# Performance work log

Measured on AMD Instinct MI355X. Metric: run time of the kernel, lower is better.

The kernel has to match this reference:

```python
import jax, jax.numpy as jnp
import numpy as np

H, W, CIN = 448, 608, 64
D = (128, 128, 1024)  # depth list from the module
SCALE = 0.02

def setup_inputs() -> dict:
    key = jax.random.key(0)
    ks = jax.random.split(key, 9)
    f32 = jnp.float32
    return {
        "x":  jax.random.normal(ks[0], (1, CIN, H, W), f32),
        "w1": jax.random.normal(ks[1], (D[0], CIN, 3, 3), f32) * SCALE,
        "b1": jax.random.normal(ks[2], (D[0],), f32) * SCALE,
        "w2": jax.random.normal(ks[3], (H, D[1], D[0]), f32) * SCALE,
        "b2": jax.random.normal(ks[4], (H, D[1]), f32) * SCALE,
        "w3": jax.random.normal(ks[5], (H, D[2], D[1]), f32) * SCALE,
        "b3": jax.random.normal(ks[6], (H, D[2]), f32) * SCALE,
        "w4": jax.random.normal(ks[7], (H, 2, D[2]), f32) * SCALE,
        "b4": jax.random.normal(ks[8], (H, 2), f32) * SCALE,
    }

def _lrelu(v):
    return jax.nn.leaky_relu(v, 0.01)  # PyTorch F.leaky_relu default slope

def reference(x, w1, b1, w2, b2, w3, b3, w4, b4):
    # stage_1: 3x3 conv, padding=1, + leaky_relu   -> [B,128,H,W]
    y = jax.lax.conv_general_dilated(
        x, w1, window_strides=(1, 1), padding='SAME',
        dimension_numbers=('NCHW', 'OIHW', 'NCHW'))
    y = _lrelu(y + b1[None, :, None, None])
    # transpose(1,2) + reshape -> grouped 1x1 convs (groups=H) == per-row GEMMs
    y = jnp.transpose(y, (0, 2, 1, 3))                      # [B,H,128,W]
    y = _lrelu(jnp.einsum('bhcw,hdc->bhdw', y, w2) + b2[None, :, :, None])
    y = _lrelu(jnp.einsum('bhcw,hdc->bhdw', y, w3) + b3[None, :, :, None])
    y = jnp.einsum('bhcw,hdc->bhdw', y, w4) + b4[None, :, :, None]  # [B,H,2,W]
    y = jnp.transpose(y, (0, 2, 1, 3))                      # [B,2,H,W]
    out = y[:, 0]
    mask = _lrelu(y[:, 1])   # mask branch      [B,H,W]
    return (out, mask)
```

## Files before the change

kernel.cpp:

```cpp
#include <hip/hip_runtime.h>

#define HH 448
#define WW 608
#define D1 128
#define D2 128
#define D3 1024
#define HWPROD (HH*WW)
#define CLW 164

typedef __bf16 bf16x8 __attribute__((ext_vector_type(8)));
typedef float  f32x4  __attribute__((ext_vector_type(4)));
typedef _Float16 f16x4 __attribute__((ext_vector_type(4)));

__device__ inline unsigned short f2bf(float v) {
    __bf16 b = (__bf16)v;
    return __builtin_bit_cast(unsigned short, b);
}

__device__ inline bf16x8 cvt8c(const float* __restrict__ p) {
    f32x4 f0 = *reinterpret_cast<const f32x4*>(p);
    f32x4 f1 = *reinterpret_cast<const f32x4*>(p + 4);
    bf16x8 r;
    r[0]=(__bf16)f0[0]; r[1]=(__bf16)f0[1]; r[2]=(__bf16)f0[2]; r[3]=(__bf16)f0[3];
    r[4]=(__bf16)f1[0]; r[5]=(__bf16)f1[1]; r[6]=(__bf16)f1[2]; r[7]=(__bf16)f1[3];
    return r;
}

__global__ __launch_bounds__(256) void transpose_x_kernel(
    const float* __restrict__ x, unsigned short* __restrict__ xt)
{
    const int pos = blockIdx.x * 256 + threadIdx.x;
    #pragma unroll
    for (int c8 = 0; c8 < 8; ++c8) {
        bf16x8 r;
        #pragma unroll
        for (int j = 0; j < 8; ++j)
            r[j] = (__bf16)x[(size_t)(c8 * 8 + j) * HWPROD + pos];
        *reinterpret_cast<bf16x8*>(xt + (size_t)pos * 64 + c8 * 8) = r;
    }
}

__global__ __launch_bounds__(256) void convert_w1_kernel(
    const float* __restrict__ w1, unsigned short* __restrict__ w1t)
{
    const int idx = blockIdx.x * 256 + threadIdx.x;
    if (idx >= 9 * D1 * 64) return;
    const int tap = idx / (D1 * 64);
    const int rem = idx - tap * (D1 * 64);
    const int d = rem >> 6, c = rem & 63;
    w1t[idx] = f2bf(w1[(d * 64 + c) * 9 + tap]);
}

__global__ __launch_bounds__(512) void conv_kernel(
    const unsigned short* __restrict__ xt, const unsigned short* __restrict__ w1t,
    const float* __restrict__ b1, unsigned short* __restrict__ y1)
{
    __shared__ __align__(16) unsigned char lds[3 * CLW * 128];
    const int h      = blockIdx.y;
    const int wstart = blockIdx.x * 152;
    const int tid  = threadIdx.x;
    const int lane = tid & 63, wv = tid >> 6;
    const int l15 = lane & 15, lg = lane >> 4;
    const int wd = wv >> 2, wn = wv & 3;
    const int d0 = wd * 64;
    const int start = (wn < 2) ? wn * 3 : 6 + (wn - 2) * 2;
    const int cnt   = (wn < 2) ? 3 : 2;

    for (int i = 0; i < 8; ++i) {
        const int s = i * 512 + tid;
        if (s < 3 * CLW * 8) {
            const int slot = s & 7;
            const int rw   = s >> 3;
            const int ri   = rw / CLW;
            const int wl   = rw - ri * CLW;
            const int hs   = h + ri - 1;
            const int gw   = wstart + wl - 1;
            uint4 val = {0u, 0u, 0u, 0u};
            if ((unsigned)hs < (unsigned)HH && (unsigned)gw < (unsigned)WW)
                val = *reinterpret_cast<const uint4*>(xt + ((size_t)hs * WW + gw) * 64 + slot * 8);
            const int dslot = slot ^ (rw & 7);
            *reinterpret_cast<uint4*>(&lds[(size_t)rw * 128 + dslot * 16]) = val;
        }
    }

    f32x4 b1v[4];
    #pragma unroll
    for (int mf = 0; mf < 4; ++mf)
        b1v[mf] = *reinterpret_cast<const f32x4*>(b1 + d0 + mf * 16 + lg * 4);
    f32x4 acc[3][4];
    #pragma unroll
    for (int f = 0; f < 3; ++f)
        #pragma unroll
        for (int mf = 0; mf < 4; ++mf)
            acc[f][mf] = b1v[mf];

    __syncthreads();

    #pragma unroll
    for (int tap = 0; tap < 9; ++tap) {
        const int ty = tap / 3, tx = tap - ty * 3;
        bf16x8 a[4][2];
        #pragma unroll
        for (int mf = 0; mf < 4; ++mf)
            #pragma unroll
            for (int kc = 0; kc < 2; ++kc)
                a[mf][kc] = *reinterpret_cast<const bf16x8*>(
                    w1t + ((size_t)(tap * D1 + d0 + mf * 16 + l15)) * 64 + kc * 32 + lg * 8);
        #pragma unroll
        for (int f = 0; f < 3; ++f) {
            if (f < cnt) {
                const int col = (start + f) * 16 + l15;
                const int row = ty * CLW + col + tx;
                bf16x8 b[2];
                #pragma unroll
                for (int kc = 0; kc < 2; ++kc) {
                    const int sl = (kc * 4 + lg) ^ (row & 7);
                    b[kc] = *reinterpret_cast<const bf16x8*>(&lds[(size_t)row * 128 + sl * 16]);
                }
                #pragma unroll
                for (int mf = 0; mf < 4; ++mf)
                    #pragma unroll
                    for (int kc = 0; kc < 2; ++kc)
                        acc[f][mf] = __builtin_amdgcn_mfma_f32_16x16x32_bf16(
                            a[mf][kc], b[kc], acc[f][mf], 0, 0, 0);
            }
        }
    }

    #pragma unroll
    for (int f = 0; f < 3; ++f) {
        if (f < cnt) {
            const int wl = (start + f) * 16 + l15;
            if (wl < 152) {
                const int w = wstart + wl;
                #pragma unroll
                for (int mf = 0; mf < 4; ++mf) {
                    ushort4 o;
                    #pragma unroll
                    for (int r = 0; r < 4; ++r) {
                        float v = acc[f][mf][r];
                        v = fmaxf(v, 0.01f * v);
                        ((unsigned short*)&o)[r] = f2bf(v);
                    }
                    *reinterpret_cast<ushort4*>(
                        y1 + ((size_t)h * WW + w) * D1 + d0 + mf * 16 + lg * 4) = o;
                }
            }
        }
    }
}

__device__ inline void decode_pair(int bid, int& h, int& half) {
    const int s = bid & 7, j = bid >> 3;
    half = j & 1;
    h = (j >> 1) * 8 + s;
}

__global__ __launch_bounds__(512) void gemm2_kernel(
    const unsigned short* __restrict__ y1, const float* __restrict__ w2,
    const float* __restrict__ b2, unsigned short* __restrict__ y2)
{
    __shared__ __align__(16) unsigned char lds[312 * 256];
    int h, half;
    decode_pair(blockIdx.x, h, half);
    const int wstart = half * 304;
    const int tid = threadIdx.x;
    const int lane = tid & 63, wv = tid >> 6;
    const int l15 = lane & 15, lg = lane >> 4;
    const int rw = (wv & 3) * 32;
    const int cs = (wv >> 2) * 152;

    {
        const unsigned char* src = reinterpret_cast<const unsigned char*>(
            y1 + ((size_t)h * WW + wstart) * D1);
        #pragma unroll
        for (int i = 0; i < 10; ++i) {
            const int c16 = i * 512 + tid;
            if (c16 < 304 * 16) {
                const int byte = c16 * 16;
                const int row  = byte >> 8;
                const int slot = (byte >> 4) & 15;
                uint4 val = *reinterpret_cast<const uint4*>(src + byte);
                *reinterpret_cast<uint4*>(&lds[row * 256 + ((slot ^ (row & 15)) << 4)]) = val;
            }
        }
    }

    bf16x8 a[2][4];
    #pragma unroll
    for (int mf = 0; mf < 2; ++mf)
        #pragma unroll
        for (int kc = 0; kc < 4; ++kc)
            a[mf][kc] = cvt8c(w2 + ((size_t)h * D2 + rw + mf * 16 + l15) * D1 + kc * 32 + lg * 8);
    f32x4 b2v[2];
    #pragma unroll
    for (int mf = 0; mf < 2; ++mf)
        b2v[mf] = *reinterpret_cast<const f32x4*>(b2 + (size_t)h * D2 + rw + mf * 16 + lg * 4);

    const int csw = (cs + l15) & 15;
    int boff[4];
    #pragma unroll
    for (int kc = 0; kc < 4; ++kc)
        boff[kc] = ((kc * 4 + lg) ^ csw) << 4;

    __syncthreads();

    for (int nf = 0; nf < 10; ++nf) {
        const int col = cs + nf * 16 + l15;
        bf16x8 b[4];
        #pragma unroll
        for (int kc = 0; kc < 4; ++kc)
            b[kc] = *reinterpret_cast<const bf16x8*>(&lds[col * 256 + boff[kc]]);
        f32x4 t[2] = {b2v[0], b2v[1]};
        #pragma unroll
        for (int kc = 0; kc < 4; ++kc) {
            t[0] = __builtin_amdgcn_mfma_f32_16x16x32_bf16(a[0][kc], b[kc], t[0], 0, 0, 0);
            t[1] = __builtin_amdgcn_mfma_f32_16x16x32_bf16(a[1][kc], b[kc], t[1], 0, 0, 0);
        }
        if (col < cs + 152) {
            #pragma unroll
            for (int mf = 0; mf < 2; ++mf) {
                ushort4 o;
                #pragma unroll
                for (int r = 0; r < 4; ++r) {
                    float v = t[mf][r];
                    v = fmaxf(v, 0.01f * v);
                    ((unsigned short*)&o)[r] = f2bf(v);
                }
                *reinterpret_cast<ushort4*>(
                    y2 + ((size_t)h * WW + wstart + col) * D2 + rw + mf * 16 + lg * 4) = o;
            }
        }
    }
}

__global__ __launch_bounds__(512) void gemm3_kernel(
    const unsigned short* __restrict__ y2, const float* __restrict__ w3,
    const float* __restrict__ b3, const float* __restrict__ w4,
    const float* __restrict__ b4, float* __restrict__ out)
{
    __shared__ __align__(16) unsigned char lds[304 * 256 + 2 * 304 * 4];
    float* pk = reinterpret_cast<float*>(&lds[304 * 256]);
    int h, half;
    decode_pair(blockIdx.x, h, half);
    const int wstart = half * 304;
    const int tid = threadIdx.x;
    const int lane = tid & 63, wv = tid >> 6;
    const int l15 = lane & 15, lg = lane >> 4;
    const int e0 = wv * 128;

    for (int i = tid; i < 2 * 304; i += 512) pk[i] = 0.f;

    {
        const unsigned char* src = reinterpret_cast<const unsigned char*>(
            y2 + ((size_t)h * WW + wstart) * D2);
        #pragma unroll
        for (int i = 0; i < 10; ++i) {
            const int c16 = i * 512 + tid;
            if (c16 < 304 * 16) {
                const int byte = c16 * 16;
                const int row  = byte >> 8;
                const int slot = (byte >> 4) & 15;
                uint4 val = *reinterpret_cast<const uint4*>(src + byte);
                *reinterpret_cast<uint4*>(&lds[row * 256 + ((slot ^ (row & 15)) << 4)]) = val;
            }
        }
    }

    int boff[4];
    #pragma unroll
    for (int kc = 0; kc < 4; ++kc)
        boff[kc] = l15 * 256 + (((kc * 4 + lg) ^ l15) << 4);

    bf16x8 a[4][4];
    f32x4 b3v[4];
    f16x4 af[4];
    {
        const int e64 = e0;
        #pragma unroll
        for (int mf = 0; mf < 4; ++mf) {
            #pragma unroll
            for (int kc = 0; kc < 4; ++kc)
                a[mf][kc] = cvt8c(w3 + ((size_t)h * D3 + e64 + mf * 16 + l15) * D2 + kc * 32 + lg * 8);
            b3v[mf] = *reinterpret_cast<const f32x4*>(b3 + (size_t)h * D3 + e64 + mf * 16 + lg * 4);
            f16x4 z = {(_Float16)0.f, (_Float16)0.f, (_Float16)0.f, (_Float16)0.f};
            if (l15 < 2) {
                f32x4 wv4 = *reinterpret_cast<const f32x4*>(
                    w4 + (size_t)h * 2 * D3 + (size_t)l15 * D3 + e64 + mf * 16 + lg * 4);
                #pragma unroll
                for (int j = 0; j < 4; ++j) z[j] = (_Float16)wv4[j];
            }
            af[mf] = z;
        }
    }

    __syncthreads();

    #pragma unroll 1
    for (int ct = 0; ct < 2; ++ct) {
        if (ct == 1) {
            const int e64 = e0 + 64;
            #pragma unroll
            for (int mf = 0; mf < 4; ++mf) {
                #pragma unroll
                for (int kc = 0; kc < 4; ++kc)
                    a[mf][kc] = cvt8c(w3 + ((size_t)h * D3 + e64 + mf * 16 + l15) * D2 + kc * 32 + lg * 8);
                b3v[mf] = *reinterpret_cast<const f32x4*>(b3 + (size_t)h * D3 + e64 + mf * 16 + lg * 4);
                f16x4 z = {(_Float16)0.f, (_Float16)0.f, (_Float16)0.f, (_Float16)0.f};
                if (l15 < 2) {
                    f32x4 wv4 = *reinterpret_cast<const f32x4*>(
                        w4 + (size_t)h * 2 * D3 + (size_t)l15 * D3 + e64 + mf * 16 + lg * 4);
                    #pragma unroll
                    for (int j = 0; j < 4; ++j) z[j] = (_Float16)wv4[j];
                }
                af[mf] = z;
            }
        }

        for (int nf = 0; nf < 19; ++nf) {
            bf16x8 b[4];
            #pragma unroll
            for (int kc = 0; kc < 4; ++kc)
                b[kc] = *reinterpret_cast<const bf16x8*>(&lds[nf * 4096 + boff[kc]]);
            f32x4 t[4] = {b3v[0], b3v[1], b3v[2], b3v[3]};
            #pragma unroll
            for (int kc = 0; kc < 4; ++kc)
                #pragma unroll
                for (int mf = 0; mf < 4; ++mf)
                    t[mf] = __builtin_amdgcn_mfma_f32_16x16x32_bf16(a[mf][kc], b[kc], t[mf], 0, 0, 0);

            f32x4 pacc = {};
            #pragma unroll
            for (int mf = 0; mf < 4; ++mf) {
                f16x4 vb;
                #pragma unroll
                for (int r = 0; r < 4; ++r) {
                    float v = fmaxf(t[mf][r], 0.01f * t[mf][r]);
                    vb[r] = (_Float16)v;
                }
                pacc = __builtin_amdgcn_mfma_f32_16x16x16f16(af[mf], vb, pacc, 0, 0, 0);
            }
            if (lg == 0) {
                atomicAdd(&pk[nf * 16 + l15], pacc[0]);
                atomicAdd(&pk[304 + nf * 16 + l15], pacc[1]);
            }
        }
    }
    __syncthreads();

    const float bb0 = b4[h * 2 + 0], bb1 = b4[h * 2 + 1];
    if (tid < 304) {
        float s0 = pk[tid] + bb0;
        float s1 = pk[304 + tid] + bb1;
        out[(size_t)h * WW + wstart + tid] = s0;
        out[(size_t)HWPROD + (size_t)h * WW + wstart + tid] = fmaxf(s1, 0.01f * s1);
    }
}

extern "C" void kernel_launch(void* const* d_in, const int* in_sizes, int n_in,
                              void* d_out, int out_size, void* d_ws, size_t ws_size,
                              hipStream_t stream) {
    const float* x  = (const float*)d_in[0];
    const float* w1 = (const float*)d_in[1];
    const float* b1 = (const float*)d_in[2];
    const float* w2 = (const float*)d_in[3];
    const float* b2 = (const float*)d_in[4];
    const float* w3 = (const float*)d_in[5];
    const float* b3 = (const float*)d_in[6];
    const float* w4 = (const float*)d_in[7];
    const float* b4 = (const float*)d_in[8];
    float* out = (float*)d_out;

    char* ws = (char*)d_ws;
    size_t off = 0;
    unsigned short* y1 = (unsigned short*)(ws + off); off += (size_t)HWPROD * D1 * 2;
    char* regionB = ws + off; off += (size_t)HWPROD * D2 * 2;
    unsigned short* xt = (unsigned short*)regionB;
    unsigned short* y2 = (unsigned short*)regionB;
    unsigned short* w1t = (unsigned short*)(ws + off); off += (size_t)9 * D1 * 64 * 2;

    transpose_x_kernel<<<HWPROD / 256, 256, 0, stream>>>(x, xt);
    convert_w1_kernel<<<(9 * D1 * 64 + 255) / 256, 256, 0, stream>>>(w1, w1t);

    conv_kernel <<<dim3(4, HH), 512, 0, stream>>>(xt, w1t, b1, y1);
    gemm2_kernel<<<896, 512, 0, stream>>>(y1, w2, b2, y2);
    gemm3_kernel<<<896, 512, 0, stream>>>(y2, w3, b3, w4, b4, out);
}
```

Before: 361.9 us.

## Process full rows in gemm3 and pre-convert w3 to bf16 in gemm2

gemm3 now runs one block per row h over all 608 columns instead of two half-row blocks. Each w3 slice is therefore loaded once per row rather than twice, at the cost of fewer blocks (448) and a larger LDS footprint of about 160 KB. gemm2 also converts its row's w3 slice to bf16 into a workspace buffer when the workspace is large enough, so gemm3 reads half the bytes and skips the conversion. The trade is extra writes in gemm2 and lower occupancy/parallelism in gemm3.

```diff
diff --git a/kernel.cpp b/kernel.cpp
--- a/kernel.cpp
+++ b/kernel.cpp
@@ -158,7 +158,8 @@
 
 __global__ __launch_bounds__(512) void gemm2_kernel(
     const unsigned short* __restrict__ y1, const float* __restrict__ w2,
-    const float* __restrict__ b2, unsigned short* __restrict__ y2)
+    const float* __restrict__ b2, unsigned short* __restrict__ y2,
+    const float* __restrict__ w3, unsigned short* __restrict__ w3b, int do_cvt)
 {
     __shared__ __align__(16) unsigned char lds[312 * 256];
     int h, half;
@@ -232,40 +233,44 @@
             }
         }
     }
-}
-
+
+    if (do_cvt) {
+        const size_t base = (size_t)h * (D3 * D2) + (size_t)half * (512 * D2);
+        #pragma unroll
+        for (int it = 0; it < 16; ++it) {
+            const size_t idx = base + ((size_t)(it * 512 + tid)) * 8;
+            *reinterpret_cast<bf16x8*>(w3b + idx) = cvt8c(w3 + idx);
+        }
+    }
+}
+
+template<bool W3BF16>
 __global__ __launch_bounds__(512) void gemm3_kernel(
-    const unsigned short* __restrict__ y2, const float* __restrict__ w3,
+    const unsigned short* __restrict__ y2, const void* __restrict__ w3v,
     const float* __restrict__ b3, const float* __restrict__ w4,
     const float* __restrict__ b4, float* __restrict__ out)
 {
-    __shared__ __align__(16) unsigned char lds[304 * 256 + 2 * 304 * 4];
-    float* pk = reinterpret_cast<float*>(&lds[304 * 256]);
-    int h, half;
-    decode_pair(blockIdx.x, h, half);
-    const int wstart = half * 304;
+    __shared__ __align__(16) unsigned char lds[WW * 256 + 2 * WW * 4];
+    float* pk = reinterpret_cast<float*>(&lds[WW * 256]);
+    const int h = blockIdx.x;
     const int tid = threadIdx.x;
     const int lane = tid & 63, wv = tid >> 6;
     const int l15 = lane & 15, lg = lane >> 4;
     const int e0 = wv * 128;
 
-    for (int i = tid; i < 2 * 304; i += 512) pk[i] = 0.f;
-
     {
         const unsigned char* src = reinterpret_cast<const unsigned char*>(
-            y2 + ((size_t)h * WW + wstart) * D2);
-        #pragma unroll
-        for (int i = 0; i < 10; ++i) {
-            const int c16 = i * 512 + tid;
-            if (c16 < 304 * 16) {
-                const int byte = c16 * 16;
-                const int row  = byte >> 8;
-                const int slot = (byte >> 4) & 15;
-                uint4 val = *reinterpret_cast<const uint4*>(src + byte);
-                *reinterpret_cast<uint4*>(&lds[row * 256 + ((slot ^ (row & 15)) << 4)]) = val;
-            }
-        }
-    }
+            y2 + (size_t)h * WW * D2);
+        #pragma unroll
+        for (int i = 0; i < 19; ++i) {
+            const int byte = (i * 512 + tid) * 16;
+            const int row  = byte >> 8;
+            const int slot = (byte >> 4) & 15;
+            uint4 val = *reinterpret_cast<const uint4*>(src + byte);
+            *reinterpret_cast<uint4*>(&lds[row * 256 + ((slot ^ (row & 15)) << 4)]) = val;
+        }
+    }
+    for (int i = tid; i < 2 * WW; i += 512) pk[i] = 0.f;
 
     int boff[4];
     #pragma unroll
@@ -275,23 +280,28 @@
     bf16x8 a[4][4];
     f32x4 b3v[4];
     f16x4 af[4];
-    {
-        const int e64 = e0;
-        #pragma unroll
-        for (int mf = 0; mf < 4; ++mf) {
-            #pragma unroll
-            for (int kc = 0; kc < 4; ++kc)
-                a[mf][kc] = cvt8c(w3 + ((size_t)h * D3 + e64 + mf * 16 + l15) * D2 + kc * 32 + lg * 8);
-            b3v[mf] = *reinterpret_cast<const f32x4*>(b3 + (size_t)h * D3 + e64 + mf * 16 + lg * 4);
-            f16x4 z = {(_Float16)0.f, (_Float16)0.f, (_Float16)0.f, (_Float16)0.f};
-            if (l15 < 2) {
-                f32x4 wv4 = *reinterpret_cast<const f32x4*>(
-                    w4 + (size_t)h * 2 * D3 + (size_t)l15 * D3 + e64 + mf * 16 + lg * 4);
-                #pragma unroll
-                for (int j = 0; j < 4; ++j) z[j] = (_Float16)wv4[j];
-            }
-            af[mf] = z;
-        }
+    #pragma unroll
+    for (int mf = 0; mf < 4; ++mf) {
+        #pragma unroll
+        for (int kc = 0; kc < 4; ++kc) {
+            if constexpr (W3BF16) {
+                const unsigned short* w3b = (const unsigned short*)w3v;
+                a[mf][kc] = *reinterpret_cast<const bf16x8*>(
+                    w3b + ((size_t)h * D3 + e0 + mf * 16 + l15) * D2 + kc * 32 + lg * 8);
+            } else {
+                const float* w3 = (const float*)w3v;
+                a[mf][kc] = cvt8c(w3 + ((size_t)h * D3 + e0 + mf * 16 + l15) * D2 + kc * 32 + lg * 8);
+            }
+        }
+        b3v[mf] = *reinterpret_cast<const f32x4*>(b3 + (size_t)h * D3 + e0 + mf * 16 + lg * 4);
+        f16x4 z = {(_Float16)0.f, (_Float16)0.f, (_Float16)0.f, (_Float16)0.f};
+        if (l15 < 2) {
+            f32x4 wv4 = *reinterpret_cast<const f32x4*>(
+                w4 + (size_t)h * 2 * D3 + (size_t)l15 * D3 + e0 + mf * 16 + lg * 4);
+            #pragma unroll
+            for (int j = 0; j < 4; ++j) z[j] = (_Float16)wv4[j];
+        }
+        af[mf] = z;
     }
 
     __syncthreads();
@@ -303,8 +313,16 @@
             #pragma unroll
             for (int mf = 0; mf < 4; ++mf) {
                 #pragma unroll
-                for (int kc = 0; kc < 4; ++kc)
-                    a[mf][kc] = cvt8c(w3 + ((size_t)h * D3 + e64 + mf * 16 + l15) * D2 + kc * 32 + lg * 8);
+                for (int kc = 0; kc < 4; ++kc) {
+                    if constexpr (W3BF16) {
+                        const unsigned short* w3b = (const unsigned short*)w3v;
+                        a[mf][kc] = *reinterpret_cast<const bf16x8*>(
+                            w3b + ((size_t)h * D3 + e64 + mf * 16 + l15) * D2 + kc * 32 + lg * 8);
+                    } else {
+                        const float* w3 = (const float*)w3v;
+                        a[mf][kc] = cvt8c(w3 + ((size_t)h * D3 + e64 + mf * 16 + l15) * D2 + kc * 32 + lg * 8);
+                    }
+                }
                 b3v[mf] = *reinterpret_cast<const f32x4*>(b3 + (size_t)h * D3 + e64 + mf * 16 + lg * 4);
                 f16x4 z = {(_Float16)0.f, (_Float16)0.f, (_Float16)0.f, (_Float16)0.f};
                 if (l15 < 2) {
@@ -317,7 +335,7 @@
             }
         }
 
-        for (int nf = 0; nf < 19; ++nf) {
+        for (int nf = 0; nf < 38; ++nf) {
             bf16x8 b[4];
             #pragma unroll
             for (int kc = 0; kc < 4; ++kc)
@@ -342,18 +360,18 @@
             }
             if (lg == 0) {
                 atomicAdd(&pk[nf * 16 + l15], pacc[0]);
-                atomicAdd(&pk[304 + nf * 16 + l15], pacc[1]);
+                atomicAdd(&pk[WW + nf * 16 + l15], pacc[1]);
             }
         }
     }
     __syncthreads();
 
     const float bb0 = b4[h * 2 + 0], bb1 = b4[h * 2 + 1];
-    if (tid < 304) {
-        float s0 = pk[tid] + bb0;
-        float s1 = pk[304 + tid] + bb1;
-        out[(size_t)h * WW + wstart + tid] = s0;
-        out[(size_t)HWPROD + (size_t)h * WW + wstart + tid] = fmaxf(s1, 0.01f * s1);
+    for (int i = tid; i < WW; i += 512) {
+        float s0 = pk[i] + bb0;
+        float s1 = pk[WW + i] + bb1;
+        out[(size_t)h * WW + i] = s0;
+        out[(size_t)HWPROD + (size_t)h * WW + i] = fmaxf(s1, 0.01f * s1);
     }
 }
 
@@ -378,11 +396,17 @@
     unsigned short* xt = (unsigned short*)regionB;
     unsigned short* y2 = (unsigned short*)regionB;
     unsigned short* w1t = (unsigned short*)(ws + off); off += (size_t)9 * D1 * 64 * 2;
+    unsigned short* w3b = (unsigned short*)(ws + off);
+    const size_t w3b_bytes = (size_t)HH * D3 * D2 * 2;
+    const bool use_bf16 = (ws_size >= off + w3b_bytes);
 
     transpose_x_kernel<<<HWPROD / 256, 256, 0, stream>>>(x, xt);
     convert_w1_kernel<<<(9 * D1 * 64 + 255) / 256, 256, 0, stream>>>(w1, w1t);
 
     conv_kernel <<<dim3(4, HH), 512, 0, stream>>>(xt, w1t, b1, y1);
-    gemm2_kernel<<<896, 512, 0, stream>>>(y1, w2, b2, y2);
-    gemm3_kernel<<<896, 512, 0, stream>>>(y2, w3, b3, w4, b4, out);
-}
+    gemm2_kernel<<<896, 512, 0, stream>>>(y1, w2, b2, y2, w3, w3b, use_bf16 ? 1 : 0);
+    if (use_bf16)
+        gemm3_kernel<true><<<HH, 512, 0, stream>>>(y2, w3b, b3, w4, b4, out);
+    else
+        gemm3_kernel<false><<<HH, 512, 0, stream>>>(y2, w3, b3, w4, b4, out);
+}
```

After: 387.7 us. 1.07x slower.

## Read conv and gemm3 B operands from global memory; split gemm3 over output channels

Applied to the files above, without the earlier changes.

The conv kernel no longer stages the haloed input rows in LDS. Each wave now loads its B fragments directly from global memory, with per-tap bounds checks, which removes the staging loop and the barrier. gemm3 is restructured so each block handles a full row and a quarter of the 1024 output channels (1792 blocks). B fragments are read straight from global memory instead of through swizzled LDS, and each block writes per-quarter partial sums to a workspace that a new final kernel reduces and finishes with bias and activation. This adds parallelism and cuts per-block register pressure, but it relies on cache for operand reuse, adds a partial-sum round trip through global memory, and adds an extra launch.

```diff
diff --git a/kernel.cpp b/kernel.cpp
--- a/kernel.cpp
+++ b/kernel.cpp
@@ -6,7 +6,6 @@
 #define D2 128
 #define D3 1024
 #define HWPROD (HH*WW)
-#define CLW 164
 
 typedef __bf16 bf16x8 __attribute__((ext_vector_type(8)));
 typedef float  f32x4  __attribute__((ext_vector_type(4)));
@@ -26,6 +25,13 @@
     return r;
 }
 
+__device__ inline bf16x8 zero8() {
+    bf16x8 r;
+    #pragma unroll
+    for (int j = 0; j < 8; ++j) r[j] = (__bf16)0.f;
+    return r;
+}
+
 __global__ __launch_bounds__(256) void transpose_x_kernel(
     const float* __restrict__ x, unsigned short* __restrict__ xt)
 {
@@ -55,7 +61,6 @@
     const unsigned short* __restrict__ xt, const unsigned short* __restrict__ w1t,
     const float* __restrict__ b1, unsigned short* __restrict__ y1)
 {
-    __shared__ __align__(16) unsigned char lds[3 * CLW * 128];
     const int h      = blockIdx.y;
     const int wstart = blockIdx.x * 152;
     const int tid  = threadIdx.x;
@@ -66,23 +71,6 @@
     const int start = (wn < 2) ? wn * 3 : 6 + (wn - 2) * 2;
     const int cnt   = (wn < 2) ? 3 : 2;
 
-    for (int i = 0; i < 8; ++i) {
-        const int s = i * 512 + tid;
-        if (s < 3 * CLW * 8) {
-            const int slot = s & 7;
-            const int rw   = s >> 3;
-            const int ri   = rw / CLW;
-            const int wl   = rw - ri * CLW;
-            const int hs   = h + ri - 1;
-            const int gw   = wstart + wl - 1;
-            uint4 val = {0u, 0u, 0u, 0u};
-            if ((unsigned)hs < (unsigned)HH && (unsigned)gw < (unsigned)WW)
-                val = *reinterpret_cast<const uint4*>(xt + ((size_t)hs * WW + gw) * 64 + slot * 8);
-            const int dslot = slot ^ (rw & 7);
-            *reinterpret_cast<uint4*>(&lds[(size_t)rw * 128 + dslot * 16]) = val;
-        }
-    }
-
     f32x4 b1v[4];
     #pragma unroll
     for (int mf = 0; mf < 4; ++mf)
@@ -94,11 +82,11 @@
         for (int mf = 0; mf < 4; ++mf)
             acc[f][mf] = b1v[mf];
 
-    __syncthreads();
-
     #pragma unroll
     for (int tap = 0; tap < 9; ++tap) {
         const int ty = tap / 3, tx = tap - ty * 3;
+        const int hs = h + ty - 1;
+        const bool hok = (unsigned)hs < (unsigned)HH;
         bf16x8 a[4][2];
         #pragma unroll
         for (int mf = 0; mf < 4; ++mf)
@@ -109,14 +97,14 @@
         #pragma unroll
         for (int f = 0; f < 3; ++f) {
             if (f < cnt) {
-                const int col = (start + f) * 16 + l15;
-                const int row = ty * CLW + col + tx;
+                const int wsrc = wstart + (start + f) * 16 + l15 + tx - 1;
+                const bool ok = hok && (unsigned)wsrc < (unsigned)WW;
                 bf16x8 b[2];
                 #pragma unroll
-                for (int kc = 0; kc < 2; ++kc) {
-                    const int sl = (kc * 4 + lg) ^ (row & 7);
-                    b[kc] = *reinterpret_cast<const bf16x8*>(&lds[(size_t)row * 128 + sl * 16]);
-                }
+                for (int kc = 0; kc < 2; ++kc)
+                    b[kc] = ok ? *reinterpret_cast<const bf16x8*>(
+                                     xt + ((size_t)hs * WW + wsrc) * 64 + kc * 32 + lg * 8)
+                               : zero8();
                 #pragma unroll
                 for (int mf = 0; mf < 4; ++mf)
                     #pragma unroll
@@ -237,123 +225,95 @@
 __global__ __launch_bounds__(512) void gemm3_kernel(
     const unsigned short* __restrict__ y2, const float* __restrict__ w3,
     const float* __restrict__ b3, const float* __restrict__ w4,
-    const float* __restrict__ b4, float* __restrict__ out)
-{
-    __shared__ __align__(16) unsigned char lds[304 * 256 + 2 * 304 * 4];
-    float* pk = reinterpret_cast<float*>(&lds[304 * 256]);
-    int h, half;
-    decode_pair(blockIdx.x, h, half);
-    const int wstart = half * 304;
+    float* __restrict__ part)
+{
+    __shared__ float pk[2 * WW];
+    int h, q;
+    { const int s = blockIdx.x & 7, j = blockIdx.x >> 3; q = j & 3; h = (j >> 2) * 8 + s; }
     const int tid = threadIdx.x;
     const int lane = tid & 63, wv = tid >> 6;
     const int l15 = lane & 15, lg = lane >> 4;
-    const int e0 = wv * 128;
-
-    for (int i = tid; i < 2 * 304; i += 512) pk[i] = 0.f;
-
+    const int e_base = q * 256 + wv * 32;
+
+    for (int i = tid; i < 2 * WW; i += 512) pk[i] = 0.f;
+
+    bf16x8 a0[4], a1[4];
+    #pragma unroll
+    for (int kc = 0; kc < 4; ++kc)
+        a0[kc] = cvt8c(w3 + ((size_t)h * D3 + e_base + l15) * D2 + kc * 32 + lg * 8);
+    #pragma unroll
+    for (int kc = 0; kc < 4; ++kc)
+        a1[kc] = cvt8c(w3 + ((size_t)h * D3 + e_base + 16 + l15) * D2 + kc * 32 + lg * 8);
+    f32x4 b30 = *reinterpret_cast<const f32x4*>(b3 + (size_t)h * D3 + e_base + lg * 4);
+    f32x4 b31 = *reinterpret_cast<const f32x4*>(b3 + (size_t)h * D3 + e_base + 16 + lg * 4);
+    f16x4 af0, af1;
     {
-        const unsigned char* src = reinterpret_cast<const unsigned char*>(
-            y2 + ((size_t)h * WW + wstart) * D2);
-        #pragma unroll
-        for (int i = 0; i < 10; ++i) {
-            const int c16 = i * 512 + tid;
-            if (c16 < 304 * 16) {
-                const int byte = c16 * 16;
-                const int row  = byte >> 8;
-                const int slot = (byte >> 4) & 15;
-                uint4 val = *reinterpret_cast<const uint4*>(src + byte);
-                *reinterpret_cast<uint4*>(&lds[row * 256 + ((slot ^ (row & 15)) << 4)]) = val;
-            }
-        }
-    }
-
-    int boff[4];
-    #pragma unroll
-    for (int kc = 0; kc < 4; ++kc)
-        boff[kc] = l15 * 256 + (((kc * 4 + lg) ^ l15) << 4);
-
-    bf16x8 a[4][4];
-    f32x4 b3v[4];
-    f16x4 af[4];
-    {
-        const int e64 = e0;
-        #pragma unroll
-        for (int mf = 0; mf < 4; ++mf) {
+        f16x4 z0 = {(_Float16)0.f, (_Float16)0.f, (_Float16)0.f, (_Float16)0.f};
+        f16x4 z1 = z0;
+        if (l15 < 2) {
+            f32x4 w0 = *reinterpret_cast<const f32x4*>(
+                w4 + (size_t)h * 2 * D3 + (size_t)l15 * D3 + e_base + lg * 4);
+            f32x4 w1v = *reinterpret_cast<const f32x4*>(
+                w4 + (size_t)h * 2 * D3 + (size_t)l15 * D3 + e_base + 16 + lg * 4);
             #pragma unroll
-            for (int kc = 0; kc < 4; ++kc)
-                a[mf][kc] = cvt8c(w3 + ((size_t)h * D3 + e64 + mf * 16 + l15) * D2 + kc * 32 + lg * 8);
-            b3v[mf] = *reinterpret_cast<const f32x4*>(b3 + (size_t)h * D3 + e64 + mf * 16 + lg * 4);
-            f16x4 z = {(_Float16)0.f, (_Float16)0.f, (_Float16)0.f, (_Float16)0.f};
-            if (l15 < 2) {
-                f32x4 wv4 = *reinterpret_cast<const f32x4*>(
-                    w4 + (size_t)h * 2 * D3 + (size_t)l15 * D3 + e64 + mf * 16 + lg * 4);
-                #pragma unroll
-                for (int j = 0; j < 4; ++j) z[j] = (_Float16)wv4[j];
-            }
-            af[mf] = z;
-        }
+            for (int j = 0; j < 4; ++j) { z0[j] = (_Float16)w0[j]; z1[j] = (_Float16)w1v[j]; }
+        }
+        af0 = z0; af1 = z1;
     }
 
     __syncthreads();
 
-    #pragma unroll 1
-    for (int ct = 0; ct < 2; ++ct) {
-        if (ct == 1) {
-            const int e64 = e0 + 64;
-            #pragma unroll
-            for (int mf = 0; mf < 4; ++mf) {
-                #pragma unroll
-                for (int kc = 0; kc < 4; ++kc)
-                    a[mf][kc] = cvt8c(w3 + ((size_t)h * D3 + e64 + mf * 16 + l15) * D2 + kc * 32 + lg * 8);
-                b3v[mf] = *reinterpret_cast<const f32x4*>(b3 + (size_t)h * D3 + e64 + mf * 16 + lg * 4);
-                f16x4 z = {(_Float16)0.f, (_Float16)0.f, (_Float16)0.f, (_Float16)0.f};
-                if (l15 < 2) {
-                    f32x4 wv4 = *reinterpret_cast<const f32x4*>(
-                        w4 + (size_t)h * 2 * D3 + (size_t)l15 * D3 + e64 + mf * 16 + lg * 4);
-                    #pragma unroll
-                    for (int j = 0; j < 4; ++j) z[j] = (_Float16)wv4[j];
-                }
-                af[mf] = z;
-            }
-        }
-
-        for (int nf = 0; nf < 19; ++nf) {
-            bf16x8 b[4];
-            #pragma unroll
-            for (int kc = 0; kc < 4; ++kc)
-                b[kc] = *reinterpret_cast<const bf16x8*>(&lds[nf * 4096 + boff[kc]]);
-            f32x4 t[4] = {b3v[0], b3v[1], b3v[2], b3v[3]};
-            #pragma unroll
-            for (int kc = 0; kc < 4; ++kc)
-                #pragma unroll
-                for (int mf = 0; mf < 4; ++mf)
-                    t[mf] = __builtin_amdgcn_mfma_f32_16x16x32_bf16(a[mf][kc], b[kc], t[mf], 0, 0, 0);
-
-            f32x4 pacc = {};
-            #pragma unroll
-            for (int mf = 0; mf < 4; ++mf) {
-                f16x4 vb;
-                #pragma unroll
-                for (int r = 0; r < 4; ++r) {
-                    float v = fmaxf(t[mf][r], 0.01f * t[mf][r]);
-                    vb[r] = (_Float16)v;
-                }
-                pacc = __builtin_amdgcn_mfma_f32_16x16x16f16(af[mf], vb, pacc, 0, 0, 0);
-            }
-            if (lg == 0) {
-                atomicAdd(&pk[nf * 16 + l15], pacc[0]);
-                atomicAdd(&pk[304 + nf * 16 + l15], pacc[1]);
-            }
+    const unsigned short* __restrict__ y2h = y2 + (size_t)h * WW * D2;
+    for (int nf = 0; nf < 38; ++nf) {
+        const int col = nf * 16 + l15;
+        const unsigned short* bp = y2h + (size_t)col * D2 + lg * 8;
+        bf16x8 b[4];
+        #pragma unroll
+        for (int kc = 0; kc < 4; ++kc)
+            b[kc] = *reinterpret_cast<const bf16x8*>(bp + kc * 32);
+        f32x4 t0 = b30, t1 = b31;
+        #pragma unroll
+        for (int kc = 0; kc < 4; ++kc) {
+            t0 = __builtin_amdgcn_mfma_f32_16x16x32_bf16(a0[kc], b[kc], t0, 0, 0, 0);
+            t1 = __builtin_amdgcn_mfma_f32_16x16x32_bf16(a1[kc], b[kc], t1, 0, 0, 0);
+        }
+        f16x4 v0, v1;
+        #pragma unroll
+        for (int r = 0; r < 4; ++r) {
+            v0[r] = (_Float16)fmaxf(t0[r], 0.01f * t0[r]);
+            v1[r] = (_Float16)fmaxf(t1[r], 0.01f * t1[r]);
+        }
+        f32x4 p = {};
+        p = __builtin_amdgcn_mfma_f32_16x16x16f16(af0, v0, p, 0, 0, 0);
+        p = __builtin_amdgcn_mfma_f32_16x16x16f16(af1, v1, p, 0, 0, 0);
+        if (lg == 0) {
+            atomicAdd(&pk[col], p[0]);
+            atomicAdd(&pk[WW + col], p[1]);
         }
     }
     __syncthreads();
 
-    const float bb0 = b4[h * 2 + 0], bb1 = b4[h * 2 + 1];
-    if (tid < 304) {
-        float s0 = pk[tid] + bb0;
-        float s1 = pk[304 + tid] + bb1;
-        out[(size_t)h * WW + wstart + tid] = s0;
-        out[(size_t)HWPROD + (size_t)h * WW + wstart + tid] = fmaxf(s1, 0.01f * s1);
+    for (int i = tid; i < WW; i += 512) {
+        part[(((size_t)h * 4 + q) * 2 + 0) * WW + i] = pk[i];
+        part[(((size_t)h * 4 + q) * 2 + 1) * WW + i] = pk[WW + i];
+    }
+}
+
+__global__ __launch_bounds__(640) void final_kernel(
+    const float* __restrict__ part, const float* __restrict__ b4,
+    float* __restrict__ out)
+{
+    const int h = blockIdx.x;
+    const int w = threadIdx.x;
+    if (w < WW) {
+        float s0 = b4[h * 2 + 0], s1 = b4[h * 2 + 1];
+        #pragma unroll
+        for (int q = 0; q < 4; ++q) {
+            s0 += part[(((size_t)h * 4 + q) * 2 + 0) * WW + w];
+            s1 += part[(((size_t)h * 4 + q) * 2 + 1) * WW + w];
+        }
+        out[(size_t)h * WW + w] = s0;
+        out[(size_t)HWPROD + (size_t)h * WW + w] = fmaxf(s1, 0.01f * s1);
     }
 }
 
@@ -378,11 +338,13 @@
     unsigned short* xt = (unsigned short*)regionB;
     unsigned short* y2 = (unsigned short*)regionB;
     unsigned short* w1t = (unsigned short*)(ws + off); off += (size_t)9 * D1 * 64 * 2;
+    float* part = (float*)(ws + off); off += (size_t)HH * 4 * 2 * WW * 4;
 
     transpose_x_kernel<<<HWPROD / 256, 256, 0, stream>>>(x, xt);
     convert_w1_kernel<<<(9 * D1 * 64 + 255) / 256, 256, 0, stream>>>(w1, w1t);
 
     conv_kernel <<<dim3(4, HH), 512, 0, stream>>>(xt, w1t, b1, y1);
     gemm2_kernel<<<896, 512, 0, stream>>>(y1, w2, b2, y2);
-    gemm3_kernel<<<896, 512, 0, stream>>>(y2, w3, b3, w4, b4, out);
-}
+    gemm3_kernel<<<1792, 512, 0, stream>>>(y2, w3, b3, w4, part);
+    final_kernel<<<HH, 640, 0, stream>>>(part, b4, out);
+}
```

Measured after the change: 571.1 us. 57.8% more time.

## Double block size for conv and gemm3 to cover full rows per block

Applied to the files above, without the earlier changes.

The conv kernel now uses 1024-thread blocks covering 304 columns, so half as many blocks reload the halo. The fused gemm3/gemm4 kernel now processes a whole image row per 1024-thread block, with 16 waves each owning 64 output channels, so w3 weights are loaded and converted once per row instead of being reloaded per half-row and per channel tile. The goal is less redundant weight traffic and more reuse of the staged activations. In exchange, the larger LDS footprint (about 160KB in gemm3) and higher register pressure from 1024-thread launch bounds leave one block per CU with 448 blocks, which may lower occupancy and latency hiding.

```diff
diff --git a/kernel.cpp b/kernel.cpp
--- a/kernel.cpp
+++ b/kernel.cpp
@@ -6,7 +6,7 @@
 #define D2 128
 #define D3 1024
 #define HWPROD (HH*WW)
-#define CLW 164
+#define CLW3 306
 
 typedef __bf16 bf16x8 __attribute__((ext_vector_type(8)));
 typedef float  f32x4  __attribute__((ext_vector_type(4)));
@@ -51,28 +51,29 @@
     w1t[idx] = f2bf(w1[(d * 64 + c) * 9 + tap]);
 }
 
-__global__ __launch_bounds__(512) void conv_kernel(
+__global__ __launch_bounds__(1024) void conv_kernel(
     const unsigned short* __restrict__ xt, const unsigned short* __restrict__ w1t,
     const float* __restrict__ b1, unsigned short* __restrict__ y1)
 {
-    __shared__ __align__(16) unsigned char lds[3 * CLW * 128];
+    __shared__ __align__(16) unsigned char lds[3 * CLW3 * 128];
     const int h      = blockIdx.y;
-    const int wstart = blockIdx.x * 152;
+    const int wstart = blockIdx.x * 304;
     const int tid  = threadIdx.x;
     const int lane = tid & 63, wv = tid >> 6;
     const int l15 = lane & 15, lg = lane >> 4;
-    const int wd = wv >> 2, wn = wv & 3;
+    const int wd = wv >> 3, wn = wv & 7;
     const int d0 = wd * 64;
-    const int start = (wn < 2) ? wn * 3 : 6 + (wn - 2) * 2;
-    const int cnt   = (wn < 2) ? 3 : 2;
-
+    const int start = (wn < 3) ? wn * 3 : 9 + (wn - 3) * 2;
+    const int cnt   = (wn < 3) ? 3 : 2;
+
+    #pragma unroll
     for (int i = 0; i < 8; ++i) {
-        const int s = i * 512 + tid;
-        if (s < 3 * CLW * 8) {
+        const int s = i * 1024 + tid;
+        if (s < 3 * CLW3 * 8) {
             const int slot = s & 7;
             const int rw   = s >> 3;
-            const int ri   = rw / CLW;
-            const int wl   = rw - ri * CLW;
+            const int ri   = (rw >= 2 * CLW3) ? 2 : ((rw >= CLW3) ? 1 : 0);
+            const int wl   = rw - ri * CLW3;
             const int hs   = h + ri - 1;
             const int gw   = wstart + wl - 1;
             uint4 val = {0u, 0u, 0u, 0u};
@@ -110,7 +111,7 @@
         for (int f = 0; f < 3; ++f) {
             if (f < cnt) {
                 const int col = (start + f) * 16 + l15;
-                const int row = ty * CLW + col + tx;
+                const int row = ty * CLW3 + col + tx;
                 bf16x8 b[2];
                 #pragma unroll
                 for (int kc = 0; kc < 2; ++kc) {
@@ -130,21 +131,18 @@
     #pragma unroll
     for (int f = 0; f < 3; ++f) {
         if (f < cnt) {
-            const int wl = (start + f) * 16 + l15;
-            if (wl < 152) {
-                const int w = wstart + wl;
+            const int w = wstart + (start + f) * 16 + l15;
+            #pragma unroll
+            for (int mf = 0; mf < 4; ++mf) {
+                ushort4 o;
                 #pragma unroll
-                for (int mf = 0; mf < 4; ++mf) {
-                    ushort4 o;
-                    #pragma unroll
-                    for (int r = 0; r < 4; ++r) {
-                        float v = acc[f][mf][r];
-                        v = fmaxf(v, 0.01f * v);
-                        ((unsigned short*)&o)[r] = f2bf(v);
-                    }
-                    *reinterpret_cast<ushort4*>(
-                        y1 + ((size_t)h * WW + w) * D1 + d0 + mf * 16 + lg * 4) = o;
+                for (int r = 0; r < 4; ++r) {
+                    float v = acc[f][mf][r];
+                    v = fmaxf(v, 0.01f * v);
+                    ((unsigned short*)&o)[r] = f2bf(v);
                 }
+                *reinterpret_cast<ushort4*>(
+                    y1 + ((size_t)h * WW + w) * D1 + d0 + mf * 16 + lg * 4) = o;
             }
         }
     }
@@ -234,30 +232,45 @@
     }
 }
 
-__global__ __launch_bounds__(512) void gemm3_kernel(
+__global__ __launch_bounds__(1024) void gemm3_kernel(
     const unsigned short* __restrict__ y2, const float* __restrict__ w3,
     const float* __restrict__ b3, const float* __restrict__ w4,
     const float* __restrict__ b4, float* __restrict__ out)
 {
-    __shared__ __align__(16) unsigned char lds[304 * 256 + 2 * 304 * 4];
-    float* pk = reinterpret_cast<float*>(&lds[304 * 256]);
-    int h, half;
-    decode_pair(blockIdx.x, h, half);
-    const int wstart = half * 304;
+    __shared__ __align__(16) unsigned char lds[WW * 256 + 2 * WW * 4];
+    float* pk = reinterpret_cast<float*>(&lds[WW * 256]);
+    const int h = blockIdx.x;
     const int tid = threadIdx.x;
     const int lane = tid & 63, wv = tid >> 6;
     const int l15 = lane & 15, lg = lane >> 4;
-    const int e0 = wv * 128;
-
-    for (int i = tid; i < 2 * 304; i += 512) pk[i] = 0.f;
+    const int e0 = wv * 64;
+
+    bf16x8 a[4][4];
+    f32x4 b3v[4];
+    f16x4 af[4];
+    #pragma unroll
+    for (int mf = 0; mf < 4; ++mf) {
+        #pragma unroll
+        for (int kc = 0; kc < 4; ++kc)
+            a[mf][kc] = cvt8c(w3 + ((size_t)h * D3 + e0 + mf * 16 + l15) * D2 + kc * 32 + lg * 8);
+        b3v[mf] = *reinterpret_cast<const f32x4*>(b3 + (size_t)h * D3 + e0 + mf * 16 + lg * 4);
+        f16x4 z = {(_Float16)0.f, (_Float16)0.f, (_Float16)0.f, (_Float16)0.f};
+        if (l15 < 2) {
+            f32x4 wv4 = *reinterpret_cast<const f32x4*>(
+                w4 + (size_t)h * 2 * D3 + (size_t)l15 * D3 + e0 + mf * 16 + lg * 4);
+            #pragma unroll
+            for (int j = 0; j < 4; ++j) z[j] = (_Float16)wv4[j];
+        }
+        af[mf] = z;
+    }
 
     {
         const unsigned char* src = reinterpret_cast<const unsigned char*>(
-            y2 + ((size_t)h * WW + wstart) * D2);
+            y2 + (size_t)h * WW * D2);
         #pragma unroll
         for (int i = 0; i < 10; ++i) {
-            const int c16 = i * 512 + tid;
-            if (c16 < 304 * 16) {
+            const int c16 = i * 1024 + tid;
+            if (c16 < WW * 16) {
                 const int byte = c16 * 16;
                 const int row  = byte >> 8;
                 const int slot = (byte >> 4) & 15;
@@ -266,94 +279,66 @@
             }
         }
     }
+    for (int i = tid; i < 2 * WW; i += 1024) pk[i] = 0.f;
 
     int boff[4];
     #pragma unroll
     for (int kc = 0; kc < 4; ++kc)
         boff[kc] = l15 * 256 + (((kc * 4 + lg) ^ l15) << 4);
 
-    bf16x8 a[4][4];
-    f32x4 b3v[4];
-    f16x4 af[4];
-    {
-        const int e64 = e0;
-        #pragma unroll
-        for (int mf = 0; mf < 4; ++mf) {
-            #pragma unroll
-            for (int kc = 0; kc < 4; ++kc)
-                a[mf][kc] = cvt8c(w3 + ((size_t)h * D3 + e64 + mf * 16 + l15) * D2 + kc * 32 + lg * 8);
-            b3v[mf] = *reinterpret_cast<const f32x4*>(b3 + (size_t)h * D3 + e64 + mf * 16 + lg * 4);
-            f16x4 z = {(_Float16)0.f, (_Float16)0.f, (_Float16)0.f, (_Float16)0.f};
-            if (l15 < 2) {
-                f32x4 wv4 = *reinterpret_cast<const f32x4*>(
-                    w4 + (size_t)h * 2 * D3 + (size_t)l15 * D3 + e64 + mf * 16 + lg * 4);
-                #pragma unroll
-                for (int j = 0; j < 4; ++j) z[j] = (_Float16)wv4[j];
-            }
-            af[mf] = z;
-        }
-    }
-
     __syncthreads();
 
-    #pragma unroll 1
-    for (int ct = 0; ct < 2; ++ct) {
-        if (ct == 1) {
-            const int e64 = e0 + 64;
-            #pragma unroll
-            for (int mf = 0; mf < 4; ++mf) {
-                #pragma unroll
-                for (int kc = 0; kc < 4; ++kc)
-                    a[mf][kc] = cvt8c(w3 + ((size_t)h * D3 + e64 + mf * 16 + l15) * D2 + kc * 32 + lg * 8);
-                b3v[mf] = *reinterpret_cast<const f32x4*>(b3 + (size_t)h * D3 + e64 + mf * 16 + lg * 4);
-                f16x4 z = {(_Float16)0.f, (_Float16)0.f, (_Float16)0.f, (_Float16)0.f};
-                if (l15 < 2) {
-                    f32x4 wv4 = *reinterpret_cast<const f32x4*>(
-                        w4 + (size_t)h * 2 * D3 + (size_t)l15 * D3 + e64 + mf * 16 + lg * 4);
-                    #pragma unroll
-                    for (int j = 0; j < 4; ++j) z[j] = (_Float16)wv4[j];
-                }
-                af[mf] = z;
-            }
-        }
-
-        for (int nf = 0; nf < 19; ++nf) {
-            bf16x8 b[4];
-            #pragma unroll
-            for (int kc = 0; kc < 4; ++kc)
-                b[kc] = *reinterpret_cast<const bf16x8*>(&lds[nf * 4096 + boff[kc]]);
-            f32x4 t[4] = {b3v[0], b3v[1], b3v[2], b3v[3]};
-            #pragma unroll
-            for (int kc = 0; kc < 4; ++kc)
-                #pragma unroll
-                for (int mf = 0; mf < 4; ++mf)
-                    t[mf] = __builtin_amdgcn_mfma_f32_16x16x32_bf16(a[mf][kc], b[kc], t[mf], 0, 0, 0);
-
-            f32x4 pacc = {};
-            #pragma unroll
-            for (int mf = 0; mf < 4; ++mf) {
-                f16x4 vb;
-                #pragma unroll
-                for (int r = 0; r < 4; ++r) {
-                    float v = fmaxf(t[mf][r], 0.01f * t[mf][r]);
-                    vb[r] = (_Float16)v;
-                }
-                pacc = __builtin_amdgcn_mfma_f32_16x16x16f16(af[mf], vb, pacc, 0, 0, 0);
-            }
-            if (lg == 0) {
-                atomicAdd(&pk[nf * 16 + l15], pacc[0]);
-                atomicAdd(&pk[304 + nf * 16 + l15], pacc[1]);
-            }
+    for (int nf = 0; nf < 38; ++nf) {
+        bf16x8 b[4];
+        #pragma unroll
+        for (int kc = 0; kc < 4; ++kc)
+            b[kc] = *reinterpret_cast<const bf16x8*>(&lds[nf * 4096 + boff[kc]]);
+
+        f32x4 pacc = {};
+        {
+            f32x4 t0 = b3v[0], t1 = b3v[1];
+            #pragma unroll
+            for (int kc = 0; kc < 4; ++kc) {
+                t0 = __builtin_amdgcn_mfma_f32_16x16x32_bf16(a[0][kc], b[kc], t0, 0, 0, 0);
+                t1 = __builtin_amdgcn_mfma_f32_16x16x32_bf16(a[1][kc], b[kc], t1, 0, 0, 0);
+            }
+            f16x4 v0, v1;
+            #pragma unroll
+            for (int r = 0; r < 4; ++r) {
+                v0[r] = (_Float16)fmaxf(t0[r], 0.01f * t0[r]);
+                v1[r] = (_Float16)fmaxf(t1[r], 0.01f * t1[r]);
+            }
+            pacc = __builtin_amdgcn_mfma_f32_16x16x16f16(af[0], v0, pacc, 0, 0, 0);
+            pacc = __builtin_amdgcn_mfma_f32_16x16x16f16(af[1], v1, pacc, 0, 0, 0);
+        }
+        {
+            f32x4 t0 = b3v[2], t1 = b3v[3];
+            #pragma unroll
+            for (int kc = 0; kc < 4; ++kc) {
+                t0 = __builtin_amdgcn_mfma_f32_16x16x32_bf16(a[2][kc], b[kc], t0, 0, 0, 0);
+                t1 = __builtin_amdgcn_mfma_f32_16x16x32_bf16(a[3][kc], b[kc], t1, 0, 0, 0);
+            }
+            f16x4 v0, v1;
+            #pragma unroll
+            for (int r = 0; r < 4; ++r) {
+                v0[r] = (_Float16)fmaxf(t0[r], 0.01f * t0[r]);
+                v1[r] = (_Float16)fmaxf(t1[r], 0.01f * t1[r]);
+            }
+            pacc = __builtin_amdgcn_mfma_f32_16x16x16f16(af[2], v0, pacc, 0, 0, 0);
+            pacc = __builtin_amdgcn_mfma_f32_16x16x16f16(af[3], v1, pacc, 0, 0, 0);
+        }
+        if (lg == 0) {
+            atomicAdd(&pk[nf * 16 + l15], pacc[0]);
+            atomicAdd(&pk[WW + nf * 16 + l15], pacc[1]);
         }
     }
     __syncthreads();
 
-    const float bb0 = b4[h * 2 + 0], bb1 = b4[h * 2 + 1];
-    if (tid < 304) {
-        float s0 = pk[tid] + bb0;
-        float s1 = pk[304 + tid] + bb1;
-        out[(size_t)h * WW + wstart + tid] = s0;
-        out[(size_t)HWPROD + (size_t)h * WW + wstart + tid] = fmaxf(s1, 0.01f * s1);
+    if (tid < WW) {
+        const float s0 = pk[tid] + b4[h * 2 + 0];
+        const float s1 = pk[WW + tid] + b4[h * 2 + 1];
+        out[(size_t)h * WW + tid] = s0;
+        out[(size_t)HWPROD + (size_t)h * WW + tid] = fmaxf(s1, 0.01f * s1);
     }
 }
 
@@ -382,7 +367,7 @@
     transpose_x_kernel<<<HWPROD / 256, 256, 0, stream>>>(x, xt);
     convert_w1_kernel<<<(9 * D1 * 64 + 255) / 256, 256, 0, stream>>>(w1, w1t);
 
-    conv_kernel <<<dim3(4, HH), 512, 0, stream>>>(xt, w1t, b1, y1);
+    conv_kernel <<<dim3(2, HH), 1024, 0, stream>>>(xt, w1t, b1, y1);
     gemm2_kernel<<<896, 512, 0, stream>>>(y1, w2, b2, y2);
-    gemm3_kernel<<<896, 512, 0, stream>>>(y2, w3, b3, w4, b4, out);
-}
+    gemm3_kernel<<<HH, 1024, 0, stream>>>(y2, w3, b3, w4, b4, out);
+}
```

Result: slower. 402.7 us (+11.3%).
